# Performance work log

Hardware: AMD Instinct MI355X
Metric: run time of the kernel (lower is better)

The kernel has to match this reference:

```python
import jax, jax.numpy as jnp
import numpy as np
import math

D_MODEL = 2048
N_HEADS = 16
D_HEAD = 128      # d_model // n_heads, also d_latent // n_heads (required by the matmul)
D_ROPE = 64
ROPE_BASE = 10000.0
B, T, PAST = 8, 4, 4092


def _rope_cos_sin(seq_len, dim, base):
    # matches precompute_freqs_cis: freqs = 1/base^(2i/dim), angles = t * freqs
    inv = 1.0 / (base ** (np.arange(0, dim, 2, dtype=np.float32) / dim))
    ang = np.outer(np.arange(seq_len, dtype=np.float32), inv)
    return jnp.asarray(np.cos(ang)), jnp.asarray(np.sin(ang))


def _apply_rope(x, cos, sin):
    # x: [B, T, H, d]; cos/sin: [T, d//2]. Complex multiply on (even, odd) pairs.
    x2 = x.reshape(x.shape[:-1] + (-1, 2))
    x0, x1 = x2[..., 0], x2[..., 1]
    c = cos[None, :, None, :]
    s = sin[None, :, None, :]
    return jnp.stack((x0 * c - x1 * s, x0 * s + x1 * c), axis=-1).reshape(x.shape)


def setup_inputs() -> dict:
    key = jax.random.key(0)
    ks = jax.random.split(key, 9)
    S = PAST + T
    hidden_states = jax.random.normal(ks[0], (B, T, D_MODEL), jnp.float32)
    c_kv_past = jax.random.normal(ks[1], (B, PAST, D_MODEL), jnp.float32)
    k_rope_past = jax.random.normal(ks[2], (B, PAST, D_ROPE), jnp.float32)
    # additive causal mask for decode: query i sits at absolute position PAST+i
    q_pos = PAST + jnp.arange(T)
    k_pos = jnp.arange(S)
    attention_mask = jnp.where(k_pos[None, :] <= q_pos[:, None], 0.0, -1e9).astype(jnp.float32)[None, None]
    w = lambda k, o, i: jax.random.normal(k, (o, i), jnp.float32) * 0.02  # torch Linear layout [out, in]
    return {
        "hidden_states": hidden_states,
        "c_kv_past": c_kv_past,
        "k_rope_past": k_rope_past,
        "attention_mask": attention_mask,
        "W_dq": w(ks[3], 512, D_MODEL),
        "W_uq_eff": w(ks[4], D_MODEL, 512),
        "W_qr": w(ks[5], N_HEADS * D_ROPE, 512),
        "W_dkv": w(ks[6], D_MODEL, D_MODEL),
        "W_kr": w(ks[7], D_ROPE, D_MODEL),
        "W_o_eff": w(ks[8], D_MODEL, D_MODEL),
    }


def reference(hidden_states, c_kv_past, k_rope_past, attention_mask,
              W_dq, W_uq_eff, W_qr, W_dkv, W_kr, W_o_eff):
    Bv, Tv, Dv = hidden_states.shape
    H, dh, dr = N_HEADS, D_HEAD, D_ROPE
    cos, sin = _rope_cos_sin(Tv, dr, ROPE_BASE)  # RoPE uses positions 0..T-1 (as in source)

    # new latent KV + rotary key (single shared rope key across heads)
    c_kv_new = hidden_states @ W_dkv.T                                   # [B,T,d_latent]
    k_rope_new = _apply_rope((hidden_states @ W_kr.T)[:, :, None, :], cos, sin)[:, :, 0, :]
    c_kv = jnp.concatenate([c_kv_past, c_kv_new], axis=1)                # [B,S,d_latent]
    k_rope = jnp.concatenate([k_rope_past, k_rope_new], axis=1)          # [B,S,dr]

    # compressed queries with absorbed up-projection
    c_q = hidden_states @ W_dq.T                                         # [B,T,d_latent_q]
    q_c = (c_q @ W_uq_eff.T).reshape(Bv, Tv, H, dh)                      # [B,T,H,dh]
    q_r = _apply_rope((c_q @ W_qr.T).reshape(Bv, Tv, H, dr), cos, sin)   # [B,T,H,dr]

    S = c_kv.shape[1]
    c_kv_heads = c_kv.reshape(Bv, S, H, dh)                              # [B,S,H,dh]
    scale = 1.0 / math.sqrt(dh + dr)
    # split-dot-product: avoids materializing the per-head expanded k_latent [B,H,S,dh+dr]
    scores = (jnp.einsum('bthd,bshd->bhts', q_c, c_kv_heads)
              + jnp.einsum('bthr,bsr->bhts', q_r, k_rope)) * scale
    scores = scores + attention_mask
    attn = jax.nn.softmax(scores, axis=-1)                               # [B,H,T,S]
    out = jnp.einsum('bhts,bshd->bthd', attn, c_kv_heads).reshape(Bv, Tv, Dv)
    output = out @ W_o_eff.T                                             # [B,T,d_model]
    return (output, c_kv, k_rope)
```

## Files before the change

### kernel.cpp

```cpp
#include <hip/hip_runtime.h>
#include <math.h>

#define NSPLIT 4
#define KB 64
#define SPLIT_KEYS 1024
#define NTILES (SPLIT_KEYS / KB)

typedef float vfloat4 __attribute__((ext_vector_type(4)));

__device__ __forceinline__ float wsum(float v) {
#pragma unroll
  for (int off = 32; off >= 1; off >>= 1) v += __shfl_xor(v, off, 64);
  return v;
}
__device__ __forceinline__ float wmax(float v) {
#pragma unroll
  for (int off = 32; off >= 1; off >>= 1) v = fmaxf(v, __shfl_xor(v, off, 64));
  return v;
}
__device__ __forceinline__ float dot4(const float4 a, const float4 b) {
  return a.x * b.x + a.y * b.y + a.z * b.z + a.w * b.w;
}

__global__ __launch_bounds__(256) void proj1_kernel(
    const float* __restrict__ hidden, const float* __restrict__ W_dq,
    const float* __restrict__ W_dkv, const float* __restrict__ W_kr,
    float* __restrict__ ws_cq, float* __restrict__ out_ckv,
    float* __restrict__ out_kr) {
  const int wave = threadIdx.x >> 6;
  const int lane = threadIdx.x & 63;
  const int jbase = (blockIdx.x * 4 + wave) * 2;
  const float* w0;
  if (jbase < 512)       w0 = W_dq  + (size_t)jbase * 2048;
  else if (jbase < 2560) w0 = W_dkv + (size_t)(jbase - 512) * 2048;
  else                   w0 = W_kr  + (size_t)(jbase - 2560) * 2048;
  const float* w1 = w0 + 2048;

  __shared__ float wlds[4][2][2048];

#pragma unroll
  for (int m = 0; m < 8; ++m) {
    __builtin_amdgcn_global_load_lds(
        (const __attribute__((address_space(1))) void*)(w0 + (m << 8) + (lane << 2)),
        (__attribute__((address_space(3))) void*)&wlds[wave][0][m << 8], 16, 0, 0);
    __builtin_amdgcn_global_load_lds(
        (const __attribute__((address_space(1))) void*)(w1 + (m << 8) + (lane << 2)),
        (__attribute__((address_space(3))) void*)&wlds[wave][1][m << 8], 16, 0, 0);
  }
  __syncthreads();

  float acc0[32], acc1[32];
#pragma unroll
  for (int i = 0; i < 32; ++i) { acc0[i] = 0.f; acc1[i] = 0.f; }

#pragma unroll 1
  for (int m = 0; m < 8; ++m) {
    const int k = (lane << 2) + (m << 8);
    const float4 wa = *(const float4*)&wlds[wave][0][k];
    const float4 wb = *(const float4*)&wlds[wave][1][k];
#pragma unroll
    for (int i = 0; i < 32; ++i) {
      const float4 a = *(const float4*)(hidden + i * 2048 + k);
      acc0[i] += dot4(a, wa);
      acc1[i] += dot4(a, wb);
    }
  }
#pragma unroll
  for (int i = 0; i < 32; ++i) { acc0[i] = wsum(acc0[i]); acc1[i] = wsum(acc1[i]); }

  if (jbase >= 2560) {
    const int r0 = jbase - 2560;
    const float inv = powf(10000.f, -(float)r0 / 64.f);
    float cs[4], sn[4];
#pragma unroll
    for (int t = 0; t < 4; ++t) { cs[t] = cosf((float)t * inv); sn[t] = sinf((float)t * inv); }
#pragma unroll
    for (int i = 0; i < 32; ++i) {
      const int t = i & 3;
      const float x0 = acc0[i], x1 = acc1[i];
      acc0[i] = x0 * cs[t] - x1 * sn[t];
      acc1[i] = x0 * sn[t] + x1 * cs[t];
    }
  }

  float myval = 0.f;
#pragma unroll
  for (int i = 0; i < 32; ++i) {
    myval = (lane == i)      ? acc0[i] : myval;
    myval = (lane == i + 32) ? acc1[i] : myval;
  }
  const int mi = lane & 31;
  const int col = jbase + (lane >> 5);
  const int b = mi >> 2, t = mi & 3;
  if (col < 512)
    ws_cq[mi * 512 + col] = myval;
  else if (col < 2560)
    out_ckv[((size_t)(b * 4096 + 4092 + t)) * 2048 + (col - 512)] = myval;
  else
    out_kr[((size_t)(b * 4096 + 4092 + t)) * 64 + (col - 2560)] = myval;
}

__global__ __launch_bounds__(256) void proj2_kernel(
    const float* __restrict__ cq, const float* __restrict__ W_uq,
    const float* __restrict__ W_qr, float* __restrict__ ws_qc,
    float* __restrict__ ws_qr) {
  const int wave = threadIdx.x >> 6;
  const int lane = threadIdx.x & 63;
  const int jbase = (blockIdx.x * 4 + wave) * 2;
  const float* w0 = (jbase < 2048) ? (W_uq + (size_t)jbase * 512)
                                   : (W_qr + (size_t)(jbase - 2048) * 512);
  const float* w1 = w0 + 512;

  __shared__ float wlds[4][2][512];

#pragma unroll
  for (int m = 0; m < 2; ++m) {
    __builtin_amdgcn_global_load_lds(
        (const __attribute__((address_space(1))) void*)(w0 + (m << 8) + (lane << 2)),
        (__attribute__((address_space(3))) void*)&wlds[wave][0][m << 8], 16, 0, 0);
    __builtin_amdgcn_global_load_lds(
        (const __attribute__((address_space(1))) void*)(w1 + (m << 8) + (lane << 2)),
        (__attribute__((address_space(3))) void*)&wlds[wave][1][m << 8], 16, 0, 0);
  }
  __syncthreads();

  float acc0[32], acc1[32];
#pragma unroll
  for (int i = 0; i < 32; ++i) { acc0[i] = 0.f; acc1[i] = 0.f; }

#pragma unroll 1
  for (int m = 0; m < 2; ++m) {
    const int k = (lane << 2) + (m << 8);
    const float4 wa = *(const float4*)&wlds[wave][0][k];
    const float4 wb = *(const float4*)&wlds[wave][1][k];
#pragma unroll
    for (int i = 0; i < 32; ++i) {
      const float4 a = *(const float4*)(cq + i * 512 + k);
      acc0[i] += dot4(a, wa);
      acc1[i] += dot4(a, wb);
    }
  }
#pragma unroll
  for (int i = 0; i < 32; ++i) { acc0[i] = wsum(acc0[i]); acc1[i] = wsum(acc1[i]); }

  if (jbase >= 2048) {
    const int r0 = (jbase - 2048) & 63;
    const float inv = powf(10000.f, -(float)r0 / 64.f);
    float cs[4], sn[4];
#pragma unroll
    for (int t = 0; t < 4; ++t) { cs[t] = cosf((float)t * inv); sn[t] = sinf((float)t * inv); }
#pragma unroll
    for (int i = 0; i < 32; ++i) {
      const int t = i & 3;
      const float x0 = acc0[i], x1 = acc1[i];
      acc0[i] = x0 * cs[t] - x1 * sn[t];
      acc1[i] = x0 * sn[t] + x1 * cs[t];
    }
  }

  float myval = 0.f;
#pragma unroll
  for (int i = 0; i < 32; ++i) {
    myval = (lane == i)      ? acc0[i] : myval;
    myval = (lane == i + 32) ? acc1[i] : myval;
  }
  const int mi = lane & 31;
  const int col = jbase + (lane >> 5);
  if (col < 2048) ws_qc[mi * 2048 + col] = myval;
  else            ws_qr[mi * 1024 + (col - 2048)] = myval;
}

__global__ __launch_bounds__(256) void rope_kernel(
    const float* __restrict__ kr_past, float* __restrict__ out_kr,
    const float* __restrict__ qr_g, float* __restrict__ rope) {
  const int chunk = blockIdx.x;
  const int b = blockIdx.y;
  const int tid = threadIdx.x;
  const int wave = tid >> 6;
  const int lane = tid & 63;
  const int s0 = chunk * 64;

  __shared__ float krt[64][68];
  __shared__ float sc[64][65];

#pragma unroll
  for (int u = 0; u < 4; ++u) {
    const int fi = tid + u * 256;
    const int row = fi >> 4;
    const int c4  = (fi & 15) << 2;
    const int s = s0 + row;
    float4 v;
    if (s < 4092) {
      v = *(const float4*)(kr_past + ((size_t)b * 4092 + s) * 64 + c4);
      *(float4*)(out_kr + ((size_t)(b * 4096 + s)) * 64 + c4) = v;
    } else {
      v = *(const float4*)(out_kr + ((size_t)(b * 4096 + s)) * 64 + c4);
    }
    *(float4*)&krt[row][c4] = v;
  }

  float4 q[16];
  {
    const float* qrp = qr_g + ((size_t)(b * 4 + (lane & 3))) * 1024 + (lane >> 2) * 64;
#pragma unroll
    for (int m = 0; m < 16; ++m) q[m] = *(const float4*)(qrp + (m << 2));
  }
  __syncthreads();

#pragma unroll 1
  for (int j = 0; j < 16; ++j) {
    const int sl = wave * 16 + j;
    float sum = 0.f;
#pragma unroll
    for (int r = 0; r < 16; ++r) {
      const float4 kv4 = *(const float4*)&krt[sl][r << 2];
      sum += dot4(q[r], kv4);
    }
    sc[lane][sl] = sum;
  }
  __syncthreads();

#pragma unroll
  for (int u = 0; u < 16; ++u) {
    const int e = tid + u * 256;
    const int ht = e >> 6, sl = e & 63;
    rope[((size_t)b * 64 + ht) * 4096 + s0 + sl] = sc[ht][sl];
  }
}

__global__ __launch_bounds__(256) void attn_kernel(
    const float* __restrict__ ckv_past, float* __restrict__ out_ckv,
    const float* __restrict__ qc_g, const float* __restrict__ rope,
    float* __restrict__ part_acc, float* __restrict__ part_ml) {
  const int sp = blockIdx.x;
  const int h  = blockIdx.y;
  const int b  = blockIdx.z;
  const int tid  = threadIdx.x;
  const int wv   = tid >> 6;
  const int lane = tid & 63;
  const int t = wv;

  __shared__ float kv[2][64][128];
  __shared__ float qc[4][128];

#pragma unroll
  for (int rep = 0; rep < 2; ++rep) {
    const int idx = tid + rep * 256;
    const int tt = idx >> 7, d = idx & 127;
    qc[tt][d] = qc_g[((size_t)(b * 4 + tt)) * 2048 + h * 128 + d];
  }

  const float* rope_pt = rope + ((size_t)b * 64 + h * 4 + t) * 4096;
  const int lim = 4092 + t;
  const int s_begin = sp * SPLIT_KEYS;

  const int lrow = lane >> 5;
  const int pos  = lane & 31;

  auto issue_tile = [&](int buf, int sbase) {
#pragma unroll
    for (int u = 0; u < 8; ++u) {
      const int row = 8 * u + 2 * wv + lrow;
      const int c = pos ^ (row & 7);
      const int s = sbase + row;
      const float* src = (s < 4092)
          ? (ckv_past + ((size_t)b * 4092 + s) * 2048 + h * 128 + (c << 2))
          : (out_ckv + ((size_t)(b * 4096 + s)) * 2048 + h * 128 + (c << 2));
      __builtin_amdgcn_global_load_lds(
          (const __attribute__((address_space(1))) void*)src,
          (__attribute__((address_space(3))) void*)&kv[buf][8 * u + 2 * wv][0],
          16, 0, 0);
    }
  };

  issue_tile(0, s_begin);
  asm volatile("s_waitcnt lgkmcnt(0)" ::: "memory");

  float m_run = -INFINITY, l_run = 0.f;
  float accX0 = 0.f, accX1 = 0.f;
  float accY0 = 0.f, accY1 = 0.f;
  float rope_cur = rope_pt[s_begin + lane];
  int cur = 0;

#pragma unroll 1
  for (int tile = 0; tile < NTILES; ++tile) {
    const int s0 = s_begin + tile * KB;
    if (tile + 1 < NTILES) issue_tile(cur ^ 1, s0 + KB);
    if (tile == 0 || tile + 1 == NTILES)
      asm volatile("s_waitcnt vmcnt(8)" ::: "memory");
    else
      asm volatile("s_waitcnt vmcnt(16)" ::: "memory");
    __builtin_amdgcn_s_barrier();

    __builtin_amdgcn_s_setprio(1);
    float rope_next = 0.f;
    if (tile + 1 < NTILES) rope_next = rope_pt[s0 + KB + lane];

    const int s = s0 + lane;
    float sc = -INFINITY;
    if (s <= lim) {
      float sumA = rope_cur, sumB = 0.f;
#pragma unroll
      for (int cc = 0; cc < 32; cc += 2) {
        const float4 kv0 = *(const float4*)&kv[cur][lane][(cc ^ (lane & 7)) << 2];
        const float4 kv1 = *(const float4*)&kv[cur][lane][((cc + 1) ^ (lane & 7)) << 2];
        sumA += dot4(kv0, *(const float4*)&qc[t][cc << 2]);
        sumB += dot4(kv1, *(const float4*)&qc[t][(cc + 1) << 2]);
      }
      sc = (sumA + sumB) * 0.07216878364870323f;
    }
    const float mt = wmax(sc);
    const float m_new = fmaxf(m_run, mt);
    const float p = expf(sc - m_new);
    const float lt = wsum(p);
    const float f = expf(m_run - m_new);
    l_run = l_run * f + lt;
    accX0 *= f; accX1 *= f; accY0 *= f; accY1 *= f;
    m_run = m_new;

    const int c0 = lane >> 1;
    const int off = (lane & 1) << 1;
    const int pu = __float_as_int(p);
#pragma unroll
    for (int kk = 0; kk < KB; kk += 2) {
      const float pv0 = __int_as_float(__builtin_amdgcn_readlane(pu, kk));
      const float pv1 = __int_as_float(__builtin_amdgcn_readlane(pu, kk + 1));
      const float2 vv0 = *(const float2*)&kv[cur][kk][((c0 ^ (kk & 7)) << 2) + off];
      const float2 vv1 = *(const float2*)&kv[cur][kk + 1][((c0 ^ ((kk + 1) & 7)) << 2) + off];
      accX0 += pv0 * vv0.x;
      accX1 += pv0 * vv0.y;
      accY0 += pv1 * vv1.x;
      accY1 += pv1 * vv1.y;
    }
    __builtin_amdgcn_s_setprio(0);

#pragma unroll
    for (int u = 0; u < 8; ++u) {
      const int fi = tid + u * 256;
      const int row = fi >> 5;
      const int c   = fi & 31;
      const int ss = s0 + row;
      if (ss < 4092) {
        const vfloat4 v = *(const vfloat4*)&kv[cur][row][(c ^ (row & 7)) << 2];
        __builtin_nontemporal_store(
            v, (vfloat4*)(out_ckv + ((size_t)(b * 4096 + ss)) * 2048 + h * 128 + (c << 2)));
      }
    }

    __builtin_amdgcn_s_barrier();
    cur ^= 1;
    rope_cur = rope_next;
  }

  const size_t base = ((size_t)((b * 16 + h) * 4 + t)) * NSPLIT + sp;
  part_acc[base * 128 + (lane << 1)]     = accX0 + accY0;
  part_acc[base * 128 + (lane << 1) + 1] = accX1 + accY1;
  if (lane == 0) {
    part_ml[base * 2]     = m_run;
    part_ml[base * 2 + 1] = l_run;
  }
}

__global__ __launch_bounds__(128) void combine_kernel(
    const float* __restrict__ part_acc, const float* __restrict__ part_ml,
    float* __restrict__ merged) {
  const int h = blockIdx.x & 15;
  const int b = blockIdx.x >> 4;
  const int d = threadIdx.x;
#pragma unroll
  for (int t = 0; t < 4; ++t) {
    const size_t base = ((size_t)((b * 16 + h) * 4 + t)) * NSPLIT;
    float mm[NSPLIT], ll[NSPLIT];
    float m = -INFINITY;
#pragma unroll
    for (int sp = 0; sp < NSPLIT; ++sp) {
      mm[sp] = part_ml[(base + sp) * 2];
      ll[sp] = part_ml[(base + sp) * 2 + 1];
      m = fmaxf(m, mm[sp]);
    }
    float den = 0.f, num = 0.f;
#pragma unroll
    for (int sp = 0; sp < NSPLIT; ++sp) {
      const float w = expf(mm[sp] - m);
      den += w * ll[sp];
      num += w * part_acc[(base + sp) * 128 + d];
    }
    merged[((size_t)(b * 4 + t)) * 2048 + h * 128 + d] = num / den;
  }
}

__global__ __launch_bounds__(256) void outproj_kernel(
    const float* __restrict__ A, const float* __restrict__ W_o,
    float* __restrict__ out0) {
  const int wave = threadIdx.x >> 6;
  const int lane = threadIdx.x & 63;
  const int jbase = (blockIdx.x * 4 + wave) * 2;
  const float* w0 = W_o + (size_t)jbase * 2048;
  const float* w1 = w0 + 2048;

  __shared__ float wlds[4][2][2048];

#pragma unroll
  for (int m = 0; m < 8; ++m) {
    __builtin_amdgcn_global_load_lds(
        (const __attribute__((address_space(1))) void*)(w0 + (m << 8) + (lane << 2)),
        (__attribute__((address_space(3))) void*)&wlds[wave][0][m << 8], 16, 0, 0);
    __builtin_amdgcn_global_load_lds(
        (const __attribute__((address_space(1))) void*)(w1 + (m << 8) + (lane << 2)),
        (__attribute__((address_space(3))) void*)&wlds[wave][1][m << 8], 16, 0, 0);
  }
  __syncthreads();

  float acc0[32], acc1[32];
#pragma unroll
  for (int i = 0; i < 32; ++i) { acc0[i] = 0.f; acc1[i] = 0.f; }

#pragma unroll 1
  for (int m = 0; m < 8; ++m) {
    const int k = (lane << 2) + (m << 8);
    const float4 wa = *(const float4*)&wlds[wave][0][k];
    const float4 wb = *(const float4*)&wlds[wave][1][k];
#pragma unroll
    for (int i = 0; i < 32; ++i) {
      const float4 a = *(const float4*)(A + i * 2048 + k);
      acc0[i] += dot4(a, wa);
      acc1[i] += dot4(a, wb);
    }
  }
#pragma unroll
  for (int i = 0; i < 32; ++i) { acc0[i] = wsum(acc0[i]); acc1[i] = wsum(acc1[i]); }
  float myval = 0.f;
#pragma unroll
  for (int i = 0; i < 32; ++i) {
    myval = (lane == i)      ? acc0[i] : myval;
    myval = (lane == i + 32) ? acc1[i] : myval;
  }
  const int mi = lane & 31;
  const int col = jbase + (lane >> 5);
  out0[(size_t)mi * 2048 + col] = myval;
}

extern "C" void kernel_launch(void* const* d_in, const int* in_sizes, int n_in,
                              void* d_out, int out_size, void* d_ws, size_t ws_size,
                              hipStream_t stream) {
  const float* hidden   = (const float*)d_in[0];
  const float* ckv_past = (const float*)d_in[1];
  const float* kr_past  = (const float*)d_in[2];
  const float* W_dq  = (const float*)d_in[4];
  const float* W_uq  = (const float*)d_in[5];
  const float* W_qr  = (const float*)d_in[6];
  const float* W_dkv = (const float*)d_in[7];
  const float* W_kr  = (const float*)d_in[8];
  const float* W_o   = (const float*)d_in[9];

  float* out0    = (float*)d_out;
  float* out_ckv = out0 + (size_t)32 * 2048;
  float* out_kr  = out_ckv + (size_t)8 * 4096 * 2048;

  float* ws       = (float*)d_ws;
  float* ws_cq    = ws;
  float* ws_qc    = ws_cq + 32 * 512;
  float* ws_qr    = ws_qc + 32 * 2048;
  float* part_acc = ws_qr + 32 * 1024;
  float* part_ml  = part_acc + (size_t)8 * 16 * 4 * NSPLIT * 128;
  float* merged   = part_ml + (size_t)8 * 16 * 4 * NSPLIT * 2;
  float* rope     = merged + 32 * 2048;

  hipLaunchKernelGGL(proj1_kernel, dim3(328), dim3(256), 0, stream,
                     hidden, W_dq, W_dkv, W_kr, ws_cq, out_ckv, out_kr);
  hipLaunchKernelGGL(proj2_kernel, dim3(384), dim3(256), 0, stream,
                     ws_cq, W_uq, W_qr, ws_qc, ws_qr);
  hipLaunchKernelGGL(rope_kernel, dim3(64, 8), dim3(256), 0, stream,
                     kr_past, out_kr, ws_qr, rope);
  hipLaunchKernelGGL(attn_kernel, dim3(NSPLIT, 16, 8), dim3(256), 0, stream,
                     ckv_past, out_ckv, ws_qc, rope, part_acc, part_ml);
  hipLaunchKernelGGL(combine_kernel, dim3(128), dim3(128), 0, stream,
                     part_acc, part_ml, merged);
  hipLaunchKernelGGL(outproj_kernel, dim3(256), dim3(256), 0, stream,
                     merged, W_o, out0);
}
```

Before: 190.9 us.

## Split c_kv cache copy into dedicated blocks interleaved with attention blocks

The attention kernel no longer writes the past c_kv tiles from shared memory to the output cache. Even-indexed blocks in a flattened grid now do a plain streaming row copy of c_kv_past into the output, while odd-indexed blocks run the split-K attention with simplified vmcnt waits. The aim is to take the store traffic off the attention critical path and spread it over more concurrent blocks. The cost is that c_kv_past is read twice, once by the copy blocks and once by the attention blocks, unless the second read hits in cache. The k_rope copy store also becomes nontemporal.

```diff
diff --git a/kernel.cpp b/kernel.cpp
--- a/kernel.cpp
+++ b/kernel.cpp
@@ -5,6 +5,7 @@
 #define KB 64
 #define SPLIT_KEYS 1024
 #define NTILES (SPLIT_KEYS / KB)
+#define NCOPYROWS 64
 
 typedef float vfloat4 __attribute__((ext_vector_type(4)));
 
@@ -192,7 +193,9 @@
     float4 v;
     if (s < 4092) {
       v = *(const float4*)(kr_past + ((size_t)b * 4092 + s) * 64 + c4);
-      *(float4*)(out_kr + ((size_t)(b * 4096 + s)) * 64 + c4) = v;
+      __builtin_nontemporal_store(
+          *(const vfloat4*)&v,
+          (vfloat4*)(out_kr + ((size_t)(b * 4096 + s)) * 64 + c4));
     } else {
       v = *(const float4*)(out_kr + ((size_t)(b * 4096 + s)) * 64 + c4);
     }
@@ -228,14 +231,36 @@
   }
 }
 
-__global__ __launch_bounds__(256) void attn_kernel(
+__global__ __launch_bounds__(256) void attn_copy_kernel(
     const float* __restrict__ ckv_past, float* __restrict__ out_ckv,
     const float* __restrict__ qc_g, const float* __restrict__ rope,
     float* __restrict__ part_acc, float* __restrict__ part_ml) {
-  const int sp = blockIdx.x;
-  const int h  = blockIdx.y;
-  const int b  = blockIdx.z;
   const int tid  = threadIdx.x;
+
+  if ((blockIdx.x & 1) == 0) {
+    const int j = blockIdx.x >> 1;
+    long r = (long)j * NCOPYROWS;
+    int b = (int)(r / 4092);
+    int s = (int)(r % 4092);
+    const int o0 = tid << 2;
+#pragma unroll 4
+    for (int rr = 0; rr < NCOPYROWS; ++rr) {
+      if (b >= 8) break;
+      const float* src = ckv_past + ((size_t)b * 4092 + s) * 2048;
+      float* dst = out_ckv + ((size_t)(b * 4096 + s)) * 2048;
+      const vfloat4 v0 = *(const vfloat4*)(src + o0);
+      const vfloat4 v1 = *(const vfloat4*)(src + o0 + 1024);
+      __builtin_nontemporal_store(v0, (vfloat4*)(dst + o0));
+      __builtin_nontemporal_store(v1, (vfloat4*)(dst + o0 + 1024));
+      if (++s == 4092) { s = 0; ++b; }
+    }
+    return;
+  }
+
+  const int idx = blockIdx.x >> 1;
+  const int sp = idx & 3;
+  const int h  = (idx >> 2) & 15;
+  const int b  = idx >> 6;
   const int wv   = tid >> 6;
   const int lane = tid & 63;
   const int t = wv;
@@ -245,8 +270,8 @@
 
 #pragma unroll
   for (int rep = 0; rep < 2; ++rep) {
-    const int idx = tid + rep * 256;
-    const int tt = idx >> 7, d = idx & 127;
+    const int idx2 = tid + rep * 256;
+    const int tt = idx2 >> 7, d = idx2 & 127;
     qc[tt][d] = qc_g[((size_t)(b * 4 + tt)) * 2048 + h * 128 + d];
   }
 
@@ -285,11 +310,12 @@
 #pragma unroll 1
   for (int tile = 0; tile < NTILES; ++tile) {
     const int s0 = s_begin + tile * KB;
-    if (tile + 1 < NTILES) issue_tile(cur ^ 1, s0 + KB);
-    if (tile == 0 || tile + 1 == NTILES)
+    if (tile + 1 < NTILES) {
+      issue_tile(cur ^ 1, s0 + KB);
       asm volatile("s_waitcnt vmcnt(8)" ::: "memory");
-    else
-      asm volatile("s_waitcnt vmcnt(16)" ::: "memory");
+    } else {
+      asm volatile("s_waitcnt vmcnt(0)" ::: "memory");
+    }
     __builtin_amdgcn_s_barrier();
 
     __builtin_amdgcn_s_setprio(1);
@@ -333,19 +359,6 @@
       accY1 += pv1 * vv1.y;
     }
     __builtin_amdgcn_s_setprio(0);
-
-#pragma unroll
-    for (int u = 0; u < 8; ++u) {
-      const int fi = tid + u * 256;
-      const int row = fi >> 5;
-      const int c   = fi & 31;
-      const int ss = s0 + row;
-      if (ss < 4092) {
-        const vfloat4 v = *(const vfloat4*)&kv[cur][row][(c ^ (row & 7)) << 2];
-        __builtin_nontemporal_store(
-            v, (vfloat4*)(out_ckv + ((size_t)(b * 4096 + ss)) * 2048 + h * 128 + (c << 2)));
-      }
-    }
 
     __builtin_amdgcn_s_barrier();
     cur ^= 1;
@@ -472,7 +485,7 @@
                      ws_cq, W_uq, W_qr, ws_qc, ws_qr);
   hipLaunchKernelGGL(rope_kernel, dim3(64, 8), dim3(256), 0, stream,
                      kr_past, out_kr, ws_qr, rope);
-  hipLaunchKernelGGL(attn_kernel, dim3(NSPLIT, 16, 8), dim3(256), 0, stream,
+  hipLaunchKernelGGL(attn_copy_kernel, dim3(1024), dim3(256), 0, stream,
                      ckv_past, out_ckv, ws_qc, rope, part_acc, part_ml);
   hipLaunchKernelGGL(combine_kernel, dim3(128), dim3(128), 0, stream,
                      part_acc, part_ml, merged);
```

Result: slower. 236.1 us (+23.7%).
